# Optimization experiments

Hardware: AMD Instinct MI355X
Metric: run time of the kernel (lower is better)

The kernel has to match this reference:

```python
import jax, jax.numpy as jnp
import numpy as np

N, E, G = 50000, 800000, 64   # nodes, edges, graphs
F, H, O = 6, 256, 2           # in_dim, hidden_dim, out_dim
NE, K, L = 8, 2, 4            # n_experts, top_k, n_layers


def setup_inputs() -> dict:
    key = jax.random.key(0)
    ks = jax.random.split(key, 12)
    s = 0.05
    return {
        "x": jax.random.normal(ks[0], (N, F), jnp.float32),
        "edge_index": jax.random.randint(ks[1], (2, E), 0, N),
        "batch": jnp.sort(jax.random.randint(ks[2], (N,), 0, G)),
        "enc_W": jax.random.normal(ks[3], (F, H), jnp.float32) * s,
        "enc_b": jnp.zeros((H,), jnp.float32),
        "rtr_W1": jax.random.normal(ks[4], (H + 2, H), jnp.float32) * s,
        "rtr_b1": jnp.zeros((H,), jnp.float32),
        "rtr_W2": jax.random.normal(ks[5], (H, NE), jnp.float32) * s,
        "rtr_b2": jnp.zeros((NE,), jnp.float32),
        "hid_Wr": jax.random.normal(ks[6], (L - 1, NE, H, H), jnp.float32) * s,
        "hid_Wn": jax.random.normal(ks[7], (L - 1, NE, H, H), jnp.float32) * s,
        "hid_b": jnp.zeros((L - 1, NE, H), jnp.float32),
        "out_Wr": jax.random.normal(ks[8], (NE, H, O), jnp.float32) * s,
        "out_Wn": jax.random.normal(ks[9], (NE, H, O), jnp.float32) * s,
        "out_b": jnp.zeros((NE, O), jnp.float32),
    }


def reference(x, edge_index, batch, enc_W, enc_b, rtr_W1, rtr_b1, rtr_W2, rtr_b2,
              hid_Wr, hid_Wn, hid_b, out_Wr, out_Wn, out_b):
    src, dst = edge_index[0], edge_index[1]

    # SharedBusEncoder: Linear + ReLU
    h = jax.nn.relu(x @ enc_W + enc_b)  # [N, H]

    # graph_size_features: per-graph node/edge counts, log-scaled, per node
    ones_n = jnp.ones((N,), h.dtype)
    nodes_per_g = jax.ops.segment_sum(ones_n, batch, num_segments=G)
    edges_per_g = jax.ops.segment_sum(jnp.ones((E,), h.dtype), batch[src], num_segments=G)
    size_feat = jnp.stack([jnp.log(nodes_per_g + 1.0)[batch],
                           jnp.log(edges_per_g + 1.0)[batch]], axis=-1)  # [N, 2]

    # BaseRouter: 2-layer MLP -> logits [N, NE]
    r = jax.nn.relu(jnp.concatenate([h, size_feat], axis=-1) @ rtr_W1 + rtr_b1)
    logits = r @ rtr_W2 + rtr_b2

    # sparse_routing (eval mode): softmax over top-k logits, scattered to dense mask
    vals, idx = jax.lax.top_k(logits, K)  # [N, K]
    w = jax.nn.softmax(vals, axis=-1)
    sparse = jnp.zeros((N, NE), h.dtype).at[jnp.arange(N)[:, None], idx].set(w)

    # Dense all-expert GraphConv stacks, mask-sum combine
    def graph_conv(he, Wr, Wn, b):
        agg = jax.ops.segment_sum(he[src], dst, num_segments=N)  # sum-aggregate neighbors
        return he @ Wr + agg @ Wn + b

    out = jnp.zeros((N, O), h.dtype)
    for e in range(NE):
        he = h
        for l in range(L - 1):
            he = jax.nn.relu(graph_conv(he, hid_Wr[l, e], hid_Wn[l, e], hid_b[l, e]))
        ye = graph_conv(he, out_Wr[e], out_Wn[e], out_b[e])  # [N, O]
        out = out + ye * sparse[:, e:e + 1]
    return out
```

## Files before the change

### kernel.cpp

```cpp
#include <hip/hip_runtime.h>
#include <cstdint>

#define NN 50000
#define EE 800000
#define GG 64

typedef unsigned short u16;
typedef __attribute__((ext_vector_type(8))) short bf16x8;
typedef __attribute__((ext_vector_type(4))) float f32x4;

__device__ __forceinline__ float bf2f(u16 v) { return __uint_as_float(((unsigned)v) << 16); }
__device__ __forceinline__ u16 f2bf(float f) {
  unsigned u = __float_as_uint(f);
  return (u16)((u + 0x7fffu + ((u >> 16) & 1u)) >> 16);
}

__device__ __forceinline__ void gload_lds16(const void* g, void* l) {
  __builtin_amdgcn_global_load_lds(
      (const __attribute__((address_space(1))) void*)g,
      (__attribute__((address_space(3))) void*)l,
      16, 0, 0);
}

__global__ void k_sentinel(float* out) { out[threadIdx.x] = 1e12f; }

__global__ __launch_bounds__(256) void k_encoder(
    const float* __restrict__ x, const float* __restrict__ W,
    const float* __restrict__ b, u16* __restrict__ hb) {
  int idx = blockIdx.x * 256 + threadIdx.x;
  if (idx >= NN * 256) return;
  int row = idx >> 8, j = idx & 255;
  float s = b[j];
#pragma unroll
  for (int k = 0; k < 6; ++k) s += x[row * 6 + k] * W[k * 256 + j];
  hb[idx] = f2bf(fmaxf(s, 0.f));
}

__global__ __launch_bounds__(256) void k_count_nodes(const int* __restrict__ batch,
                                                     int* __restrict__ ncnt) {
  int i = blockIdx.x * 256 + threadIdx.x;
  if (i < NN) atomicAdd(&ncnt[batch[i]], 1);
}

__global__ __launch_bounds__(256) void k_count_edges(const int* __restrict__ src,
                                                     const int* __restrict__ batch,
                                                     int* __restrict__ ecnt) {
  __shared__ int loc[GG];
  if (threadIdx.x < GG) loc[threadIdx.x] = 0;
  __syncthreads();
  int i = blockIdx.x * 256 + threadIdx.x;
  if (i < EE) atomicAdd(&loc[batch[src[i]]], 1);
  __syncthreads();
  if (threadIdx.x < GG) {
    int v = loc[threadIdx.x];
    if (v) atomicAdd(&ecnt[threadIdx.x], v);
  }
}

__global__ void k_log_feats(const int* __restrict__ ncnt, const int* __restrict__ ecnt,
                            float* __restrict__ gf) {
  int g = threadIdx.x;
  if (g < GG) {
    gf[g * 2] = logf((float)ncnt[g] + 1.f);
    gf[g * 2 + 1] = logf((float)ecnt[g] + 1.f);
  }
}

__global__ __launch_bounds__(256) void k_router(
    const float* __restrict__ x, const float* __restrict__ encW, const float* __restrict__ encb,
    const int* __restrict__ batch, const float* __restrict__ gf,
    const float* __restrict__ W1, const float* __restrict__ b1,
    const float* __restrict__ W2, const float* __restrict__ b2,
    float* __restrict__ sparse) {
  __shared__ float hs[8][256];
  __shared__ float rs[8][256];
  __shared__ float xv[8][6];
  __shared__ float sf[8][2];
  __shared__ float lg[8][8];
  int tid = threadIdx.x;
  int nb = blockIdx.x * 8;
  if (tid < 48) {
    int r = tid / 6, k = tid % 6;
    int node = nb + r;
    xv[r][k] = (node < NN) ? x[node * 6 + k] : 0.f;
  }
  if (tid >= 48 && tid < 56) {
    int r = tid - 48;
    int node = nb + r;
    int g = (node < NN) ? batch[node] : 0;
    sf[r][0] = gf[g * 2];
    sf[r][1] = gf[g * 2 + 1];
  }
  __syncthreads();
  {
    float wcol[6];
#pragma unroll
    for (int k = 0; k < 6; ++k) wcol[k] = encW[k * 256 + tid];
    float bb = encb[tid];
#pragma unroll
    for (int r = 0; r < 8; ++r) {
      float s = bb;
#pragma unroll
      for (int k = 0; k < 6; ++k) s += xv[r][k] * wcol[k];
      hs[r][tid] = fmaxf(s, 0.f);
    }
  }
  __syncthreads();
  float acc[8];
  float bb = b1[tid];
#pragma unroll
  for (int r = 0; r < 8; ++r) acc[r] = bb;
  for (int k = 0; k < 256; ++k) {
    float w = W1[k * 256 + tid];
#pragma unroll
    for (int r = 0; r < 8; ++r) acc[r] += hs[r][k] * w;
  }
  {
    float w0 = W1[256 * 256 + tid], w1v = W1[257 * 256 + tid];
#pragma unroll
    for (int r = 0; r < 8; ++r) acc[r] += sf[r][0] * w0 + sf[r][1] * w1v;
  }
#pragma unroll
  for (int r = 0; r < 8; ++r) rs[r][tid] = fmaxf(acc[r], 0.f);
  __syncthreads();
  if (tid < 64) {
    int r = tid >> 3, e = tid & 7;
    float s = b2[e];
    for (int k = 0; k < 256; ++k) s += rs[r][k] * W2[k * 8 + e];
    lg[r][e] = s;
  }
  __syncthreads();
  if (tid < 8) {
    int node = nb + tid;
    if (node < NN) {
      float v1 = lg[tid][0];
      int j1 = 0;
#pragma unroll
      for (int j = 1; j < 8; ++j) {
        float v = lg[tid][j];
        if (v > v1) { v1 = v; j1 = j; }
      }
      float v2 = -1e30f;
      int j2 = 0;
#pragma unroll
      for (int j = 0; j < 8; ++j) {
        if (j == j1) continue;
        float v = lg[tid][j];
        if (v > v2) { v2 = v; j2 = j; }
      }
      float ex = expf(v2 - v1);
      float wa = 1.f / (1.f + ex), wb = ex / (1.f + ex);
      float* sp = sparse + node * 8;
#pragma unroll
      for (int j = 0; j < 8; ++j) sp[j] = 0.f;
      sp[j1] = wa;
      sp[j2] = wb;
    }
  }
}

__global__ __launch_bounds__(256) void k_deg(const int* __restrict__ dst, int* __restrict__ deg) {
  int i = blockIdx.x * 256 + threadIdx.x;
  if (i < EE) atomicAdd(&deg[dst[i]], 1);
}

__global__ __launch_bounds__(1024) void k_scan(const int* __restrict__ deg,
                                               int* __restrict__ rowptr) {
  __shared__ int tmp[1024];
  __shared__ int carry;
  if (threadIdx.x == 0) { carry = 0; rowptr[0] = 0; }
  __syncthreads();
  for (int base = 0; base < NN; base += 1024) {
    int i = base + threadIdx.x;
    int v = (i < NN) ? deg[i] : 0;
    tmp[threadIdx.x] = v;
    __syncthreads();
    for (int off = 1; off < 1024; off <<= 1) {
      int t = (threadIdx.x >= off) ? tmp[threadIdx.x - off] : 0;
      __syncthreads();
      tmp[threadIdx.x] += t;
      __syncthreads();
    }
    if (i < NN) rowptr[i + 1] = carry + tmp[threadIdx.x];
    int last = tmp[1023];
    __syncthreads();
    if (threadIdx.x == 0) carry += last;
    __syncthreads();
  }
}

__global__ __launch_bounds__(256) void k_fill(const int* __restrict__ ei,
                                              const int* __restrict__ rowptr,
                                              int* __restrict__ cursor, int* __restrict__ csrc) {
  int i = blockIdx.x * 256 + threadIdx.x;
  if (i < EE) {
    int s = ei[i], d = ei[EE + i];
    int pos = atomicAdd(&cursor[d], 1);
    csrc[rowptr[d] + pos] = s;
  }
}

__global__ __launch_bounds__(256) void k_spmm256(
    const int* __restrict__ rowptr, const int* __restrict__ csrc,
    const u16* __restrict__ X, u16* __restrict__ Y) {
  int wave = threadIdx.x >> 6, lane = threadIdx.x & 63;
  int d = blockIdx.x * 4 + wave;
  if (d >= NN) return;
  int s0 = rowptr[d], s1 = rowptr[d + 1];
  int c4 = lane * 4;
  float a0 = 0.f, a1 = 0.f, a2 = 0.f, a3 = 0.f;
  int i = s0;
  for (; i + 2 <= s1; i += 2) {
    int sa = csrc[i], sb = csrc[i + 1];
    ushort4 va = *(const ushort4*)(X + sa * 256 + c4);
    ushort4 vb = *(const ushort4*)(X + sb * 256 + c4);
    a0 += bf2f(va.x) + bf2f(vb.x);
    a1 += bf2f(va.y) + bf2f(vb.y);
    a2 += bf2f(va.z) + bf2f(vb.z);
    a3 += bf2f(va.w) + bf2f(vb.w);
  }
  if (i < s1) {
    int sa = csrc[i];
    ushort4 va = *(const ushort4*)(X + sa * 256 + c4);
    a0 += bf2f(va.x);
    a1 += bf2f(va.y);
    a2 += bf2f(va.z);
    a3 += bf2f(va.w);
  }
  ushort4 o;
  o.x = f2bf(a0); o.y = f2bf(a1); o.z = f2bf(a2); o.w = f2bf(a3);
  *(ushort4*)(Y + d * 256 + c4) = o;
}

__global__ __launch_bounds__(256) void k_transpose(const float* __restrict__ W,
                                                   u16* __restrict__ Wt, int nmat) {
  int idx = blockIdx.x * 256 + threadIdx.x;
  if (idx >= nmat * 65536) return;
  int m = idx >> 16, rem = idx & 65535;
  int k = rem >> 8, j = rem & 255;
  Wt[(m << 16) + (j << 8) + k] = f2bf(W[idx]);
}

__global__ __launch_bounds__(512) void k_gemm(
    const u16* __restrict__ X1, const u16* __restrict__ X2,
    const u16* __restrict__ W1t, const u16* __restrict__ W2t,
    const float* __restrict__ bias, u16* __restrict__ Y, int relu) {
  __shared__ __align__(16) u16 Alds[128 * 32];
  __shared__ __align__(16) u16 Blds[256 * 32];
  int tid = threadIdx.x;
  int wave = tid >> 6, lane = tid & 63;
  int l15 = lane & 15, l4 = lane >> 4;
  int m0 = blockIdx.x * 128;
  int wr = wave >> 2, wc = wave & 3;
  const f32x4 fz = {0.f, 0.f, 0.f, 0.f};
  f32x4 acc[4][4];
#pragma unroll
  for (int a = 0; a < 4; ++a)
#pragma unroll
    for (int b = 0; b < 4; ++b) acc[a][b] = fz;

  for (int kt = 0; kt < 16; ++kt) {
    const u16* xs = (kt < 8) ? X1 : X2;
    const u16* wsrc = (kt < 8) ? W1t : W2t;
    int kb = (kt & 7) * 32;
    __syncthreads();
    {
      int flat = wave * 1024 + lane * 16;
      int row = flat >> 6, colb = flat & 63;
      int gr = m0 + row;
      if (gr > NN - 1) gr = NN - 1;
      gload_lds16(xs + gr * 256 + kb + (colb >> 1), (char*)Alds + wave * 1024);
    }
#pragma unroll
    for (int q = 0; q < 2; ++q) {
      int flat = q * 8192 + wave * 1024 + lane * 16;
      int row = flat >> 6, colb = flat & 63;
      gload_lds16(wsrc + row * 256 + kb + (colb >> 1), (char*)Blds + q * 8192 + wave * 1024);
    }
    __syncthreads();
    bf16x8 af[4], bfv[4];
#pragma unroll
    for (int mi = 0; mi < 4; ++mi) {
      int r = wr * 64 + mi * 16 + l15;
      af[mi] = *(const bf16x8*)(Alds + r * 32 + l4 * 8);
    }
#pragma unroll
    for (int nj = 0; nj < 4; ++nj) {
      int c = wc * 64 + nj * 16 + l15;
      bfv[nj] = *(const bf16x8*)(Blds + c * 32 + l4 * 8);
    }
#pragma unroll
    for (int mi = 0; mi < 4; ++mi)
#pragma unroll
      for (int nj = 0; nj < 4; ++nj)
        acc[mi][nj] =
            __builtin_amdgcn_mfma_f32_16x16x32_bf16(af[mi], bfv[nj], acc[mi][nj], 0, 0, 0);
  }
#pragma unroll
  for (int mi = 0; mi < 4; ++mi) {
    int rbase = m0 + wr * 64 + mi * 16 + l4 * 4;
#pragma unroll
    for (int nj = 0; nj < 4; ++nj) {
      int col = wc * 64 + nj * 16 + l15;
      float bv = bias[col];
#pragma unroll
      for (int r2 = 0; r2 < 4; ++r2) {
        int row = rbase + r2;
        if (row < NN) {
          float v = acc[mi][nj][r2] + bv;
          if (relu) v = fmaxf(v, 0.f);
          Y[row * 256 + col] = f2bf(v);
        }
      }
    }
  }
}

__global__ __launch_bounds__(256) void k_outproj(
    const u16* __restrict__ he, const float* __restrict__ Wr,
    const float* __restrict__ Wn, float* __restrict__ Y4) {
  __shared__ float Ws[256 * 4];
  int tid = threadIdx.x;
  Ws[tid * 4 + 0] = Wr[tid * 2];
  Ws[tid * 4 + 1] = Wr[tid * 2 + 1];
  Ws[tid * 4 + 2] = Wn[tid * 2];
  Ws[tid * 4 + 3] = Wn[tid * 2 + 1];
  __syncthreads();
  int wave = tid >> 6, lane = tid & 63;
  int node = blockIdx.x * 4 + wave;
  if (node >= NN) return;
  const u16* hrow = he + node * 256;
  int k0 = lane * 4;
  ushort4 hv4 = *(const ushort4*)(hrow + k0);
  float hv[4] = {bf2f(hv4.x), bf2f(hv4.y), bf2f(hv4.z), bf2f(hv4.w)};
  float a0 = 0.f, a1 = 0.f, a2 = 0.f, a3 = 0.f;
#pragma unroll
  for (int t = 0; t < 4; ++t) {
    float hvv = hv[t];
    const float* w = Ws + (k0 + t) * 4;
    a0 += hvv * w[0];
    a1 += hvv * w[1];
    a2 += hvv * w[2];
    a3 += hvv * w[3];
  }
#pragma unroll
  for (int off = 32; off > 0; off >>= 1) {
    a0 += __shfl_down(a0, off);
    a1 += __shfl_down(a1, off);
    a2 += __shfl_down(a2, off);
    a3 += __shfl_down(a3, off);
  }
  if (lane == 0) {
    float* y = Y4 + node * 4;
    y[0] = a0; y[1] = a1; y[2] = a2; y[3] = a3;
  }
}

__global__ __launch_bounds__(256) void k_out_combine(
    const int* __restrict__ rowptr, const int* __restrict__ csrc,
    const float* __restrict__ Y4, const float* __restrict__ sparse,
    const float* __restrict__ ob, float* __restrict__ out, int e) {
  int d = blockIdx.x * 256 + threadIdx.x;
  if (d >= NN) return;
  float a0 = 0.f, a1 = 0.f;
  for (int i = rowptr[d]; i < rowptr[d + 1]; ++i) {
    int s = csrc[i];
    a0 += Y4[s * 4 + 2];
    a1 += Y4[s * 4 + 3];
  }
  float w = sparse[d * 8 + e];
  out[d * 2] += w * (Y4[d * 4] + a0 + ob[0]);
  out[d * 2 + 1] += w * (Y4[d * 4 + 1] + a1 + ob[1]);
}

extern "C" void kernel_launch(void* const* d_in, const int* in_sizes, int n_in,
                              void* d_out, int out_size, void* d_ws, size_t ws_size,
                              hipStream_t stream) {
  const float* x = (const float*)d_in[0];
  const int* ei = (const int*)d_in[1];
  const int* batch = (const int*)d_in[2];
  const float* enc_W = (const float*)d_in[3];
  const float* enc_b = (const float*)d_in[4];
  const float* rW1 = (const float*)d_in[5];
  const float* rb1 = (const float*)d_in[6];
  const float* rW2 = (const float*)d_in[7];
  const float* rb2 = (const float*)d_in[8];
  const float* hid_Wr = (const float*)d_in[9];
  const float* hid_Wn = (const float*)d_in[10];
  const float* hid_b = (const float*)d_in[11];
  const float* out_Wr = (const float*)d_in[12];
  const float* out_Wn = (const float*)d_in[13];
  const float* out_b = (const float*)d_in[14];
  float* out = (float*)d_out;

  char* ws = (char*)d_ws;
  size_t off = 0;
  auto alloc = [&](size_t bytes) -> void* {
    void* p = ws + off;
    off = (off + bytes + 511) & ~(size_t)511;
    return p;
  };
  u16* hb = (u16*)alloc((size_t)NN * 256 * 2);
  u16* agg0 = (u16*)alloc((size_t)NN * 256 * 2);
  u16* he = (u16*)alloc((size_t)NN * 256 * 2);
  u16* agg = (u16*)alloc((size_t)NN * 256 * 2);
  u16* WrT = (u16*)alloc((size_t)24 * 65536 * 2);
  u16* WnT = (u16*)alloc((size_t)24 * 65536 * 2);
  int* deg = (int*)alloc((size_t)NN * 4);
  int* rowptr = (int*)alloc((size_t)(NN + 1) * 4);
  int* cursor = (int*)alloc((size_t)NN * 4);
  int* csrc = (int*)alloc((size_t)EE * 4);
  int* ncnt = (int*)alloc(GG * 4);
  int* ecnt = (int*)alloc(GG * 4);
  float* gf = (float*)alloc(GG * 2 * 4);
  float* sparse = (float*)alloc((size_t)NN * 8 * 4);
  float* Y4 = (float*)alloc((size_t)NN * 4 * 4);
  if (off > ws_size) {
    k_sentinel<<<1, 2, 0, stream>>>(out);
    return;
  }

  hipMemsetAsync(deg, 0, (size_t)NN * 4, stream);
  hipMemsetAsync(cursor, 0, (size_t)NN * 4, stream);
  hipMemsetAsync(ncnt, 0, GG * 4, stream);
  hipMemsetAsync(ecnt, 0, GG * 4, stream);
  hipMemsetAsync(out, 0, (size_t)NN * 2 * 4, stream);

  k_encoder<<<(NN * 256 + 255) / 256, 256, 0, stream>>>(x, enc_W, enc_b, hb);
  k_transpose<<<(24 * 65536 + 255) / 256, 256, 0, stream>>>(hid_Wr, WrT, 24);
  k_transpose<<<(24 * 65536 + 255) / 256, 256, 0, stream>>>(hid_Wn, WnT, 24);
  k_count_nodes<<<(NN + 255) / 256, 256, 0, stream>>>(batch, ncnt);
  k_count_edges<<<(EE + 255) / 256, 256, 0, stream>>>(ei, batch, ecnt);
  k_log_feats<<<1, 64, 0, stream>>>(ncnt, ecnt, gf);
  k_router<<<NN / 8, 256, 0, stream>>>(x, enc_W, enc_b, batch, gf, rW1, rb1, rW2, rb2, sparse);
  k_deg<<<(EE + 255) / 256, 256, 0, stream>>>(ei + EE, deg);
  k_scan<<<1, 1024, 0, stream>>>(deg, rowptr);
  k_fill<<<(EE + 255) / 256, 256, 0, stream>>>(ei, rowptr, cursor, csrc);

  const int gemm_grid = (NN + 127) / 128;
  k_spmm256<<<(NN + 3) / 4, 256, 0, stream>>>(rowptr, csrc, hb, agg0);
  for (int e = 0; e < 8; ++e) {
    k_gemm<<<gemm_grid, 512, 0, stream>>>(hb, agg0, WrT + e * 65536, WnT + e * 65536,
                                          hid_b + e * 256, he, 1);
    for (int l = 1; l < 3; ++l) {
      k_spmm256<<<(NN + 3) / 4, 256, 0, stream>>>(rowptr, csrc, he, agg);
      k_gemm<<<gemm_grid, 512, 0, stream>>>(he, agg, WrT + (l * 8 + e) * 65536,
                                            WnT + (l * 8 + e) * 65536,
                                            hid_b + (l * 8 + e) * 256, he, 1);
    }
    k_outproj<<<(NN + 3) / 4, 256, 0, stream>>>(he, out_Wr + e * 512, out_Wn + e * 512, Y4);
    k_out_combine<<<(NN + 255) / 256, 256, 0, stream>>>(rowptr, csrc, Y4, sparse,
                                                        out_b + e * 2, out, e);
  }
}
```

Before: 2.631 ms.

## Double-buffer GEMM LDS tiles with XOR swizzle and rework graph size features

The bf16 MFMA GEMM now double-buffers its A and B LDS tiles. It prefetches the next K-slice with global_load_lds while computing the current one, using an explicit vmcnt wait and barriers. An XOR swizzle on the LDS column offsets is meant to cut bank conflicts on the fragment reads. Separately, the per-graph node and edge counts now come from a per-node out-degree histogram, summed over each graph's node range found by binary search on the sorted batch array, instead of scattering every edge into the graph counters. Together these double GEMM LDS usage and rely on batch being sorted.

```diff
diff --git a/kernel.cpp b/kernel.cpp
--- a/kernel.cpp
+++ b/kernel.cpp
@@ -36,33 +36,34 @@
   hb[idx] = f2bf(fmaxf(s, 0.f));
 }
 
-__global__ __launch_bounds__(256) void k_count_nodes(const int* __restrict__ batch,
-                                                     int* __restrict__ ncnt) {
+__global__ __launch_bounds__(256) void k_outdeg(const int* __restrict__ src,
+                                                int* __restrict__ outdeg) {
   int i = blockIdx.x * 256 + threadIdx.x;
-  if (i < NN) atomicAdd(&ncnt[batch[i]], 1);
-}
-
-__global__ __launch_bounds__(256) void k_count_edges(const int* __restrict__ src,
-                                                     const int* __restrict__ batch,
-                                                     int* __restrict__ ecnt) {
-  __shared__ int loc[GG];
-  if (threadIdx.x < GG) loc[threadIdx.x] = 0;
-  __syncthreads();
-  int i = blockIdx.x * 256 + threadIdx.x;
-  if (i < EE) atomicAdd(&loc[batch[src[i]]], 1);
-  __syncthreads();
-  if (threadIdx.x < GG) {
-    int v = loc[threadIdx.x];
-    if (v) atomicAdd(&ecnt[threadIdx.x], v);
-  }
-}
-
-__global__ void k_log_feats(const int* __restrict__ ncnt, const int* __restrict__ ecnt,
-                            float* __restrict__ gf) {
-  int g = threadIdx.x;
-  if (g < GG) {
-    gf[g * 2] = logf((float)ncnt[g] + 1.f);
-    gf[g * 2 + 1] = logf((float)ecnt[g] + 1.f);
+  if (i < EE) atomicAdd(&outdeg[src[i]], 1);
+}
+
+__global__ __launch_bounds__(256) void k_graph_feats(const int* __restrict__ batch,
+                                                     const int* __restrict__ outdeg,
+                                                     float* __restrict__ gf) {
+  __shared__ int red[256];
+  int g = blockIdx.x, tid = threadIdx.x;
+  auto lb = [&](int v) {
+    int lo = 0, hi = NN;
+    while (lo < hi) { int m = (lo + hi) >> 1; if (batch[m] < v) lo = m + 1; else hi = m; }
+    return lo;
+  };
+  int bs = lb(g), be = lb(g + 1);
+  int s = 0;
+  for (int i = bs + tid; i < be; i += 256) s += outdeg[i];
+  red[tid] = s;
+  __syncthreads();
+  for (int off = 128; off > 0; off >>= 1) {
+    if (tid < off) red[tid] += red[tid + off];
+    __syncthreads();
+  }
+  if (tid == 0) {
+    gf[g * 2] = logf((float)(be - bs) + 1.f);
+    gf[g * 2 + 1] = logf((float)red[0] + 1.f);
   }
 }
 
@@ -245,8 +246,8 @@
     const u16* __restrict__ X1, const u16* __restrict__ X2,
     const u16* __restrict__ W1t, const u16* __restrict__ W2t,
     const float* __restrict__ bias, u16* __restrict__ Y, int relu) {
-  __shared__ __align__(16) u16 Alds[128 * 32];
-  __shared__ __align__(16) u16 Blds[256 * 32];
+  __shared__ __align__(16) u16 Alds[2][128 * 32];
+  __shared__ __align__(16) u16 Blds[2][256 * 32];
   int tid = threadIdx.x;
   int wave = tid >> 6, lane = tid & 63;
   int l15 = lane & 15, l4 = lane >> 4;
@@ -259,35 +260,51 @@
 #pragma unroll
     for (int b = 0; b < 4; ++b) acc[a][b] = fz;
 
-  for (int kt = 0; kt < 16; ++kt) {
-    const u16* xs = (kt < 8) ? X1 : X2;
-    const u16* wsrc = (kt < 8) ? W1t : W2t;
-    int kb = (kt & 7) * 32;
-    __syncthreads();
+  auto stage = [&](int t) {
+    const u16* xs = (t < 8) ? X1 : X2;
+    const u16* wsrc = (t < 8) ? W1t : W2t;
+    int kb = (t & 7) * 32;
+    int half = t & 1;
     {
       int flat = wave * 1024 + lane * 16;
       int row = flat >> 6, colb = flat & 63;
+      int scol = colb ^ (((row >> 1) & 3) << 4);
       int gr = m0 + row;
       if (gr > NN - 1) gr = NN - 1;
-      gload_lds16(xs + gr * 256 + kb + (colb >> 1), (char*)Alds + wave * 1024);
+      gload_lds16(xs + gr * 256 + kb + (scol >> 1), (char*)Alds[half] + flat);
     }
 #pragma unroll
     for (int q = 0; q < 2; ++q) {
       int flat = q * 8192 + wave * 1024 + lane * 16;
       int row = flat >> 6, colb = flat & 63;
-      gload_lds16(wsrc + row * 256 + kb + (colb >> 1), (char*)Blds + q * 8192 + wave * 1024);
-    }
-    __syncthreads();
+      int scol = colb ^ (((row >> 1) & 3) << 4);
+      gload_lds16(wsrc + row * 256 + kb + (scol >> 1), (char*)Blds[half] + flat);
+    }
+  };
+
+  stage(0);
+  for (int kt = 0; kt < 16; ++kt) {
+    if (kt < 15) {
+      stage(kt + 1);
+      asm volatile("s_waitcnt vmcnt(3)" ::: "memory");
+    } else {
+      asm volatile("s_waitcnt vmcnt(0)" ::: "memory");
+    }
+    __builtin_amdgcn_sched_barrier(0);
+    __builtin_amdgcn_s_barrier();
+    __builtin_amdgcn_sched_barrier(0);
+    const char* Ab = (const char*)Alds[kt & 1];
+    const char* Bb = (const char*)Blds[kt & 1];
     bf16x8 af[4], bfv[4];
 #pragma unroll
     for (int mi = 0; mi < 4; ++mi) {
       int r = wr * 64 + mi * 16 + l15;
-      af[mi] = *(const bf16x8*)(Alds + r * 32 + l4 * 8);
+      af[mi] = *(const bf16x8*)(Ab + r * 64 + ((l4 * 16) ^ (((r >> 1) & 3) << 4)));
     }
 #pragma unroll
     for (int nj = 0; nj < 4; ++nj) {
       int c = wc * 64 + nj * 16 + l15;
-      bfv[nj] = *(const bf16x8*)(Blds + c * 32 + l4 * 8);
+      bfv[nj] = *(const bf16x8*)(Bb + c * 64 + ((l4 * 16) ^ (((c >> 1) & 3) << 4)));
     }
 #pragma unroll
     for (int mi = 0; mi < 4; ++mi)
@@ -295,6 +312,8 @@
       for (int nj = 0; nj < 4; ++nj)
         acc[mi][nj] =
             __builtin_amdgcn_mfma_f32_16x16x32_bf16(af[mi], bfv[nj], acc[mi][nj], 0, 0, 0);
+    __builtin_amdgcn_sched_barrier(0);
+    __builtin_amdgcn_s_barrier();
   }
 #pragma unroll
   for (int mi = 0; mi < 4; ++mi) {
@@ -409,9 +428,8 @@
   int* deg = (int*)alloc((size_t)NN * 4);
   int* rowptr = (int*)alloc((size_t)(NN + 1) * 4);
   int* cursor = (int*)alloc((size_t)NN * 4);
+  int* outdeg = (int*)alloc((size_t)NN * 4);
   int* csrc = (int*)alloc((size_t)EE * 4);
-  int* ncnt = (int*)alloc(GG * 4);
-  int* ecnt = (int*)alloc(GG * 4);
   float* gf = (float*)alloc(GG * 2 * 4);
   float* sparse = (float*)alloc((size_t)NN * 8 * 4);
   float* Y4 = (float*)alloc((size_t)NN * 4 * 4);
@@ -422,16 +440,14 @@
 
   hipMemsetAsync(deg, 0, (size_t)NN * 4, stream);
   hipMemsetAsync(cursor, 0, (size_t)NN * 4, stream);
-  hipMemsetAsync(ncnt, 0, GG * 4, stream);
-  hipMemsetAsync(ecnt, 0, GG * 4, stream);
+  hipMemsetAsync(outdeg, 0, (size_t)NN * 4, stream);
   hipMemsetAsync(out, 0, (size_t)NN * 2 * 4, stream);
 
   k_encoder<<<(NN * 256 + 255) / 256, 256, 0, stream>>>(x, enc_W, enc_b, hb);
   k_transpose<<<(24 * 65536 + 255) / 256, 256, 0, stream>>>(hid_Wr, WrT, 24);
   k_transpose<<<(24 * 65536 + 255) / 256, 256, 0, stream>>>(hid_Wn, WnT, 24);
-  k_count_nodes<<<(NN + 255) / 256, 256, 0, stream>>>(batch, ncnt);
-  k_count_edges<<<(EE + 255) / 256, 256, 0, stream>>>(ei, batch, ecnt);
-  k_log_feats<<<1, 64, 0, stream>>>(ncnt, ecnt, gf);
+  k_outdeg<<<(EE + 255) / 256, 256, 0, stream>>>(ei, outdeg);
+  k_graph_feats<<<GG, 256, 0, stream>>>(batch, outdeg, gf);
   k_router<<<NN / 8, 256, 0, stream>>>(x, enc_W, enc_b, batch, gf, rW1, rb1, rW2, rb2, sparse);
   k_deg<<<(EE + 255) / 256, 256, 0, stream>>>(ei + EE, deg);
   k_scan<<<1, 1024, 0, stream>>>(deg, rowptr);
```

Result: slower. 2.721 ms (+3.4%).
